# Optimization experiments

Measured on AMD Instinct MI355X. Metric: run time of the kernel, lower is better.

The kernel has to match this reference:

```python
import jax, jax.numpy as jnp
import numpy as np

N, R, E, H, D_MAX = 1024, 8192, 1024, 4, 48
DH = E // H
P_EDGE = 16.0 / R  # average in-degree ~16


def setup_inputs() -> dict:
    key = jax.random.key(0)
    ks = jax.random.split(key, 6)
    s = 0.02
    return {
        "target": jax.random.normal(ks[0], (N, E), jnp.float32),
        "source": jax.random.normal(ks[1], (R, E), jnp.float32),
        "adj": (jax.random.uniform(ks[2], (N, R)) < P_EDGE).astype(jnp.float32),
        "W_trans": jax.random.normal(ks[3], (E, E), jnp.float32) * s,
        "b_trans": jnp.zeros((E,), jnp.float32),
        "in_proj_w": jax.random.normal(ks[4], (3 * E, E), jnp.float32) * s,
        "in_proj_b": jnp.zeros((3 * E,), jnp.float32),
        "out_w": jax.random.normal(ks[5], (E, E), jnp.float32) * s,
        "out_b": jnp.zeros((E,), jnp.float32),
        "unit_id": 0,
    }


def reference(target, source, adj, W_trans, b_trans, in_proj_w, in_proj_b, out_w, out_b, unit_id):
    # source = relu(trans_fc(source))
    src = jax.nn.relu(source @ W_trans.T + b_trans)  # [R, E]

    # build padded neighbor index lists (torch loops per node; here vectorized)
    deg = adj.sum(axis=1).astype(jnp.int32)                # [N]
    order = jnp.argsort(-adj, axis=1)[:, :D_MAX]           # stable: 1-columns first, ascending col idx
    valid = jnp.arange(D_MAX)[None, :] < deg[:, None]      # [N, D] True = real neighbor
    neigh = jnp.where(valid, order, 0)                     # pad with index 0 (masked, like torch)
    kv_in = src[neigh]                                     # [N, D, E] gathered neighbor feats

    # nn.MultiheadAttention: q=target (len-1 query), k=v=padded neighbors
    Wq, Wk, Wv = jnp.split(in_proj_w, 3, axis=0)
    bq, bk, bv = jnp.split(in_proj_b, 3)
    q = (target @ Wq.T + bq).reshape(-1, H, DH)            # [N, H, dh]
    k = (kv_in @ Wk.T + bk).reshape(-1, D_MAX, H, DH)      # [N, D, H, dh]
    v = (kv_in @ Wv.T + bv).reshape(-1, D_MAX, H, DH)

    scores = jnp.einsum('nhd,nkhd->nhk', q, k) / np.float32(np.sqrt(DH))  # [N, H, D]
    # key_padding_mask: padded slots -> -inf; give zero-degree nodes one dummy
    # unmasked slot so softmax stays finite (their output is zeroed below)
    safe_valid = valid.at[:, 0].set(valid[:, 0] | (deg == 0))
    scores = jnp.where(safe_valid[:, None, :], scores, -jnp.inf)
    attn = jax.nn.softmax(scores, axis=-1)
    out = jnp.einsum('nhk,nkhd->nhd', attn, v).reshape(-1, E)
    out = out @ out_w.T + out_b

    # scatter back: inactive (degree-0) nodes stay zero, like att_res_padded
    return jnp.where((deg > 0)[:, None], out, jnp.zeros((), out.dtype))
```

## Files before the change

### kernel.cpp

```cpp
#include <hip/hip_runtime.h>

#define N_NODES 1024
#define R_SRC   8192
#define E_DIM   1024
#define H_HEADS 4
#define DH_DIM  256
#define D_MAXN  48

typedef __attribute__((ext_vector_type(8))) short short8;
typedef __attribute__((ext_vector_type(4))) float f32x4;

__device__ __forceinline__ unsigned short f2bf(float f) {
    unsigned u = __float_as_uint(f);
    unsigned r = u + 0x7fffu + ((u >> 16) & 1u);
    return (unsigned short)(r >> 16);
}
__device__ __forceinline__ float bf2f(unsigned short b) {
    return __uint_as_float(((unsigned)b) << 16);
}
__device__ __forceinline__ void gload16(const void* g, void* l) {
    __builtin_amdgcn_global_load_lds(
        (const __attribute__((address_space(1))) unsigned int*)g,
        (__attribute__((address_space(3))) unsigned int*)l,
        16, 0, 0);
}
template<int N> __device__ __forceinline__ void vwait() {
    if constexpr (N == 8)       asm volatile("s_waitcnt vmcnt(8)" ::: "memory");
    else if constexpr (N == 6)  asm volatile("s_waitcnt vmcnt(6)" ::: "memory");
    else if constexpr (N == 1)  asm volatile("s_waitcnt vmcnt(1)" ::: "memory");
    else                        asm volatile("s_waitcnt vmcnt(0)" ::: "memory");
}

struct GD {
    const unsigned short* A;
    const unsigned short* B;
    const float* bias;
    void* C;
    int N, K, nbx, relu, outbf;
    const int* rowmask;
};

template<int BM, int BN>
__global__ __launch_bounds__(512) void gemm_t(GD d0, GD d1, int split)
{
    constexpr int AI = BM / 64;
    constexpr int BI = BN / 64;
    constexpr int VN = AI + BI;
    constexpr int FM = BM / 32;
    constexpr int FN = BN / 64;

    __shared__ __align__(16) unsigned short lds[3][(BM + BN) * 64];

    int bid = blockIdx.x;
    const int nwg = gridDim.x;
    bid = (bid & 7) * (nwg >> 3) + (bid >> 3);

    GD d; int q;
    if (bid < split) { d = d0; q = bid; }
    else             { d = d1; q = bid - split; }
    const int m0 = (q / d.nbx) * BM;
    const int n0 = (q % d.nbx) * BN;
    const int K  = d.K;

    const int t = threadIdx.x;
    const int w = t >> 6, l = t & 63;
    const int wm = w >> 2, wn = w & 3;

    const int trow = t >> 3, tkc = t & 7;
    const int tswz = tkc ^ (trow & 7);
    const unsigned short* gA[AI];
    const unsigned short* gB[BI];
#pragma unroll
    for (int i = 0; i < AI; ++i)
        gA[i] = d.A + (size_t)(m0 + i * 64 + trow) * K + tswz * 8;
#pragma unroll
    for (int i = 0; i < BI; ++i)
        gB[i] = d.B + (size_t)(n0 + i * 64 + trow) * K + tswz * 8;

    f32x4 acc[FM][FN] = {};

    auto STAGE = [&](int c, int kt) {
        const int ko = kt * 64;
#pragma unroll
        for (int i = 0; i < AI; ++i)
            gload16(gA[i] + ko, &lds[c][(i * 512 + t) * 8]);
#pragma unroll
        for (int i = 0; i < BI; ++i)
            gload16(gB[i] + ko, &lds[c][BM * 64 + (i * 512 + t) * 8]);
    };

    const int nt = K / 64;
    STAGE(0, 0);
    STAGE(1, 1);
    vwait<VN>();
    __builtin_amdgcn_s_barrier();

    const int lr = l & 15, hi = l >> 4;
    const int rsw = l & 7;
    const int cs0 = ((0 + hi) ^ rsw) * 8;
    const int cs1 = ((4 + hi) ^ rsw) * 8;
    const int abase = (wm * (BM / 2) + lr) * 64;
    const int bbase = BM * 64 + (wn * 64 + lr) * 64;

    for (int kt = 0; kt < nt; ++kt) {
        const int cur = kt % 3;
        if (kt + 2 < nt) STAGE((kt + 2) % 3, kt + 2);

        const unsigned short* Ls = &lds[cur][0];

        short8 bv[FN][2];
#pragma unroll
        for (int fj = 0; fj < FN; ++fj) {
            bv[fj][0] = *(const short8*)&Ls[bbase + fj * 1024 + cs0];
            bv[fj][1] = *(const short8*)&Ls[bbase + fj * 1024 + cs1];
        }
#pragma unroll
        for (int g = 0; g < FM; g += 4) {
            short8 av[4][2];
#pragma unroll
            for (int fi = 0; fi < 4; ++fi) {
                av[fi][0] = *(const short8*)&Ls[abase + (g + fi) * 1024 + cs0];
                av[fi][1] = *(const short8*)&Ls[abase + (g + fi) * 1024 + cs1];
            }
            __builtin_amdgcn_s_setprio(1);
#pragma unroll
            for (int ks = 0; ks < 2; ++ks)
#pragma unroll
                for (int fi = 0; fi < 4; ++fi)
#pragma unroll
                    for (int fj = 0; fj < FN; ++fj)
                        acc[g + fi][fj] = __builtin_amdgcn_mfma_f32_16x16x32_bf16(
                            av[fi][ks], bv[fj][ks], acc[g + fi][fj], 0, 0, 0);
            __builtin_amdgcn_s_setprio(0);
        }

        asm volatile("" ::: "memory");
        __builtin_amdgcn_s_barrier();
        if (kt + 2 < nt) {
            vwait<VN>();
        } else {
            vwait<0>();
        }
        __builtin_amdgcn_s_barrier();
    }

#pragma unroll
    for (int fj = 0; fj < FN; ++fj) {
        const int c = n0 + wn * 64 + fj * 16 + lr;
        const float bvs = d.bias[c];
#pragma unroll
        for (int fi = 0; fi < FM; ++fi) {
            const int rb = m0 + wm * (BM / 2) + fi * 16 + hi * 4;
#pragma unroll
            for (int qq = 0; qq < 4; ++qq) {
                const int r = rb + qq;
                float x = acc[fi][fj][qq] + bvs;
                if (d.relu) x = fmaxf(x, 0.0f);
                if (d.rowmask && d.rowmask[r] == 0) x = 0.0f;
                if (d.outbf) ((unsigned short*)d.C)[(size_t)r * d.N + c] = f2bf(x);
                else         ((float*)d.C)[(size_t)r * d.N + c] = x;
            }
        }
    }
}

struct GS {
    const unsigned short* A;
    const unsigned short* B;
    const float* bias;
    void* C;
    int lda, ldb, ldc, K, relu, outbf;
    long long azs, bzs, czs;
    int bias_zs;
    const int* rowmask;
};

__global__ __launch_bounds__(256) void gemm_s(GS g)
{
    const int z = blockIdx.z;
    const unsigned short* A = g.A + (size_t)((long long)z * g.azs);
    const unsigned short* B = g.B + (size_t)((long long)z * g.bzs);
    const float* bias = g.bias ? g.bias + (size_t)z * g.bias_zs : nullptr;

    __shared__ __align__(16) unsigned short S[128 * 32];

    const int t = threadIdx.x;
    const int m0 = blockIdx.y * 64;
    const int n0 = blockIdx.x * 64;
    const int w = t >> 6, l = t & 63;
    const int wrow = (w >> 1) * 32;
    const int wcol = (w & 1) * 32;
    const int lr = l & 15;
    const int kg = (l >> 4) * 8;

    f32x4 acc[2][2] = {};

    const unsigned short* gp[2];
    unsigned short* lp[2];
    {
        const int c0 = t;
        gp[0] = A + (size_t)(m0 + (c0 >> 2)) * g.lda + (c0 & 3) * 8;
        lp[0] = &S[c0 * 8];
        const int c1 = t;
        gp[1] = B + (size_t)(n0 + (c1 >> 2)) * g.ldb + (c1 & 3) * 8;
        lp[1] = &S[2048 + c1 * 8];
    }

    for (int k0 = 0; k0 < g.K; k0 += 32) {
        gload16(gp[0] + k0, lp[0]);
        gload16(gp[1] + k0, lp[1]);
        __syncthreads();

        short8 af[2], bw[2];
#pragma unroll
        for (int i = 0; i < 2; ++i)
            af[i] = *(const short8*)&S[(wrow + i * 16 + lr) * 32 + kg];
#pragma unroll
        for (int j = 0; j < 2; ++j)
            bw[j] = *(const short8*)&S[2048 + (wcol + j * 16 + lr) * 32 + kg];
#pragma unroll
        for (int i = 0; i < 2; ++i)
#pragma unroll
            for (int j = 0; j < 2; ++j)
                acc[i][j] = __builtin_amdgcn_mfma_f32_16x16x32_bf16(
                    af[i], bw[j], acc[i][j], 0, 0, 0);
        __syncthreads();
    }

#pragma unroll
    for (int j = 0; j < 2; ++j) {
        const int c = n0 + wcol + j * 16 + lr;
        const float bv = bias ? bias[c] : 0.0f;
#pragma unroll
        for (int i = 0; i < 2; ++i) {
            const int rbase = m0 + wrow + i * 16 + (l >> 4) * 4;
#pragma unroll
            for (int qq = 0; qq < 4; ++qq) {
                const int r = rbase + qq;
                float x = acc[i][j][qq] + bv;
                if (g.relu) x = fmaxf(x, 0.0f);
                if (g.rowmask && g.rowmask[r] == 0) x = 0.0f;
                if (g.outbf)
                    ((unsigned short*)g.C)[(size_t)((long long)z * g.czs) + (size_t)r * g.ldc + c] = f2bf(x);
                else
                    ((float*)g.C)[(size_t)((long long)z * g.czs) + (size_t)r * g.ldc + c] = x;
            }
        }
    }
}

struct ConvArgs {
    const float* s[4];
    unsigned short* d[4];
    unsigned off[5];
};

__global__ __launch_bounds__(256) void pre_kernel(
    const float* __restrict__ adj, int* __restrict__ neigh, int* __restrict__ deg,
    ConvArgs a, const float* __restrict__ inw_f, const float* __restrict__ tgt_f,
    const float* __restrict__ in_b, unsigned short* __restrict__ WkT,
    unsigned short* __restrict__ Q_bf, int nconv)
{
    __shared__ __align__(16) unsigned char smem[64 * 65 * 4];
    const int t = threadIdx.x;

    if (blockIdx.x < 256) {
        unsigned short (*QS)[64 * 32] = (unsigned short (*)[64 * 32])smem;
        const int qb = blockIdx.x;
        const int m0 = (qb >> 4) * 64;
        const int n0 = (qb & 15) * 64;
        const int w = t >> 6, l = t & 63;
        const int wrow = (w >> 1) * 32;
        const int wcol = (w & 1) * 32;
        const int lr = l & 15;
        const int kg = (l >> 4) * 8;
        const int row = t >> 2, k8 = (t & 3) * 8;

        const float* ga = tgt_f + (size_t)(m0 + row) * E_DIM + k8;
        const float* gb = inw_f + (size_t)(n0 + row) * E_DIM + k8;

        f32x4 acc[2][2] = {};

        for (int k0 = 0; k0 < E_DIM; k0 += 32) {
            float4 a0 = *(const float4*)(ga + k0);
            float4 a1 = *(const float4*)(ga + k0 + 4);
            float4 b0 = *(const float4*)(gb + k0);
            float4 b1 = *(const float4*)(gb + k0 + 4);
            short8 av, bv;
            av[0] = (short)f2bf(a0.x); av[1] = (short)f2bf(a0.y);
            av[2] = (short)f2bf(a0.z); av[3] = (short)f2bf(a0.w);
            av[4] = (short)f2bf(a1.x); av[5] = (short)f2bf(a1.y);
            av[6] = (short)f2bf(a1.z); av[7] = (short)f2bf(a1.w);
            bv[0] = (short)f2bf(b0.x); bv[1] = (short)f2bf(b0.y);
            bv[2] = (short)f2bf(b0.z); bv[3] = (short)f2bf(b0.w);
            bv[4] = (short)f2bf(b1.x); bv[5] = (short)f2bf(b1.y);
            bv[6] = (short)f2bf(b1.z); bv[7] = (short)f2bf(b1.w);
            *(short8*)&QS[0][row * 32 + k8] = av;
            *(short8*)&QS[1][row * 32 + k8] = bv;
            __syncthreads();

            short8 af[2], bw[2];
#pragma unroll
            for (int i = 0; i < 2; ++i)
                af[i] = *(const short8*)&QS[0][(wrow + i * 16 + lr) * 32 + kg];
#pragma unroll
            for (int j = 0; j < 2; ++j)
                bw[j] = *(const short8*)&QS[1][(wcol + j * 16 + lr) * 32 + kg];
#pragma unroll
            for (int i = 0; i < 2; ++i)
#pragma unroll
                for (int j = 0; j < 2; ++j)
                    acc[i][j] = __builtin_amdgcn_mfma_f32_16x16x32_bf16(
                        af[i], bw[j], acc[i][j], 0, 0, 0);
            __syncthreads();
        }

#pragma unroll
        for (int j = 0; j < 2; ++j) {
            const int c = n0 + wcol + j * 16 + lr;
            const float bv = in_b[c];
#pragma unroll
            for (int i = 0; i < 2; ++i) {
                const int rbase = m0 + wrow + i * 16 + (l >> 4) * 4;
#pragma unroll
                for (int qq = 0; qq < 4; ++qq)
                    Q_bf[(size_t)(rbase + qq) * E_DIM + c] = f2bf(acc[i][j][qq] + bv);
            }
        }
        return;
    }

    if (blockIdx.x < 512) {
        float (*tile)[65] = (float (*)[65])smem;
        const int tb = blockIdx.x - 256;
        const int h = tb >> 6, rem = tb & 63;
        const int e0 = (rem >> 2) * 64, d0 = (rem & 3) * 64;
        const int r = t >> 2, c4 = (t & 3) * 16;
        const float* tsrc = inw_f + (size_t)(E_DIM + h * 256 + d0 + r) * E_DIM + e0 + c4;
#pragma unroll
        for (int jj = 0; jj < 4; ++jj) {
            float4 v = ((const float4*)tsrc)[jj];
            tile[r][c4 + jj * 4 + 0] = v.x;
            tile[r][c4 + jj * 4 + 1] = v.y;
            tile[r][c4 + jj * 4 + 2] = v.z;
            tile[r][c4 + jj * 4 + 3] = v.w;
        }
        __syncthreads();
        const int er = t >> 2, dc = (t & 3) * 16;
        unsigned short* wout = WkT + ((size_t)h * E_DIM + e0 + er) * 256 + d0 + dc;
#pragma unroll
        for (int jj = 0; jj < 4; ++jj) {
            ushort4 o;
            o.x = f2bf(tile[dc + jj * 4 + 0][er]);
            o.y = f2bf(tile[dc + jj * 4 + 1][er]);
            o.z = f2bf(tile[dc + jj * 4 + 2][er]);
            o.w = f2bf(tile[dc + jj * 4 + 3][er]);
            ((ushort4*)wout)[jj] = o;
        }
        return;
    }

    if (blockIdx.x < (unsigned)(512 + N_NODES)) {
        int* s_cnt = (int*)smem;
        int (*s_idx)[D_MAXN] = (int (*)[D_MAXN])(smem + 16);

        const int n    = blockIdx.x - 512;
        const int w    = t >> 6;
        const int lane = t & 63;
        const float* row = adj + (size_t)n * R_SRC;

        const int seg0 = w * (R_SRC / 4);
        const unsigned long long lower = (1ULL << lane) - 1ULL;
        int total = 0;

        for (int base = seg0; base < seg0 + R_SRC / 4; base += 256) {
            const float v0 = row[base + lane];
            const float v1 = row[base + 64 + lane];
            const float v2 = row[base + 128 + lane];
            const float v3 = row[base + 192 + lane];
            const unsigned long long m0 = __ballot(v0 != 0.0f);
            const unsigned long long m1 = __ballot(v1 != 0.0f);
            const unsigned long long m2 = __ballot(v2 != 0.0f);
            const unsigned long long m3 = __ballot(v3 != 0.0f);
            int p;
            p = total + __popcll(m0 & lower);
            if (v0 != 0.0f && p < D_MAXN) s_idx[w][p] = base + lane;
            total += __popcll(m0);
            p = total + __popcll(m1 & lower);
            if (v1 != 0.0f && p < D_MAXN) s_idx[w][p] = base + 64 + lane;
            total += __popcll(m1);
            p = total + __popcll(m2 & lower);
            if (v2 != 0.0f && p < D_MAXN) s_idx[w][p] = base + 128 + lane;
            total += __popcll(m2);
            p = total + __popcll(m3 & lower);
            if (v3 != 0.0f && p < D_MAXN) s_idx[w][p] = base + 192 + lane;
            total += __popcll(m3);
        }
        if (lane == 0) s_cnt[w] = total;
        __syncthreads();

        int start = 0;
#pragma unroll
        for (int i = 0; i < 4; ++i) if (i < w) start += s_cnt[i];
        const int degree = s_cnt[0] + s_cnt[1] + s_cnt[2] + s_cnt[3];
        const int nstore = total < D_MAXN ? total : D_MAXN;
        if (lane < nstore) {
            const int gpos = start + lane;
            if (gpos < D_MAXN) neigh[n * D_MAXN + gpos] = s_idx[w][lane];
        }
        if (t == 0) deg[n] = degree;
        return;
    }

    unsigned i = (blockIdx.x - 512 - N_NODES) * 256 + t;
    if (i >= a.off[4]) return;
    int seg = 0;
#pragma unroll
    for (int s = 1; s < 4; ++s) seg += (i >= a.off[s]);
    unsigned j = i - a.off[seg];
    float4 v = ((const float4*)a.s[seg])[j];
    ushort4 o;
    o.x = f2bf(v.x); o.y = f2bf(v.y); o.z = f2bf(v.z); o.w = f2bf(v.w);
    ((ushort4*)a.d[seg])[j] = o;
}

__global__ __launch_bounds__(256) void gather_ctx(
    const float* __restrict__ Ahat, const unsigned short* __restrict__ srcrel,
    const int* __restrict__ neigh, const int* __restrict__ deg,
    unsigned short* __restrict__ ctx)
{
    const int n = blockIdx.x;
    const int t = threadIdx.x;
    const int h = t >> 6;
    const int lane = t & 63;

    unsigned short* crow = ctx + ((size_t)n * H_HEADS + h) * E_DIM + lane * 16;
    const int degree = deg[n];
    if (degree == 0) {
        ushort4 z4 = {0, 0, 0, 0};
#pragma unroll
        for (int j = 0; j < 4; ++j) ((ushort4*)crow)[j] = z4;
        return;
    }
    const int dv = degree < D_MAXN ? degree : D_MAXN;

    __shared__ int s_neigh[D_MAXN];
    if (t < dv) s_neigh[t] = neigh[n * D_MAXN + t];
    __syncthreads();

    float a[16];
    {
        const float4* ap = (const float4*)(Ahat + (size_t)n * (H_HEADS * E_DIM) + h * E_DIM + lane * 16);
#pragma unroll
        for (int j = 0; j < 4; ++j) {
            float4 v = ap[j];
            a[j * 4 + 0] = v.x; a[j * 4 + 1] = v.y; a[j * 4 + 2] = v.z; a[j * 4 + 3] = v.w;
        }
    }

    float m = -3.4e38f, sum = 0.0f;
    float cacc[16];
#pragma unroll
    for (int i = 0; i < 16; ++i) cacc[i] = 0.0f;

    const float scale = 0.0625f;

    int d = 0;
    for (; d + 1 < dv; d += 2) {
        const ushort4* rp0 = (const ushort4*)(srcrel + (size_t)s_neigh[d]     * E_DIM + lane * 16);
        const ushort4* rp1 = (const ushort4*)(srcrel + (size_t)s_neigh[d + 1] * E_DIM + lane * 16);
        ushort4 w00 = rp0[0], w01 = rp0[1], w02 = rp0[2], w03 = rp0[3];
        ushort4 w10 = rp1[0], w11 = rp1[1], w12 = rp1[2], w13 = rp1[3];
        float e0[16], e1[16];
        e0[0]=bf2f(w00.x); e0[1]=bf2f(w00.y); e0[2]=bf2f(w00.z); e0[3]=bf2f(w00.w);
        e0[4]=bf2f(w01.x); e0[5]=bf2f(w01.y); e0[6]=bf2f(w01.z); e0[7]=bf2f(w01.w);
        e0[8]=bf2f(w02.x); e0[9]=bf2f(w02.y); e0[10]=bf2f(w02.z); e0[11]=bf2f(w02.w);
        e0[12]=bf2f(w03.x); e0[13]=bf2f(w03.y); e0[14]=bf2f(w03.z); e0[15]=bf2f(w03.w);
        e1[0]=bf2f(w10.x); e1[1]=bf2f(w10.y); e1[2]=bf2f(w10.z); e1[3]=bf2f(w10.w);
        e1[4]=bf2f(w11.x); e1[5]=bf2f(w11.y); e1[6]=bf2f(w11.z); e1[7]=bf2f(w11.w);
        e1[8]=bf2f(w12.x); e1[9]=bf2f(w12.y); e1[10]=bf2f(w12.z); e1[11]=bf2f(w12.w);
        e1[12]=bf2f(w13.x); e1[13]=bf2f(w13.y); e1[14]=bf2f(w13.z); e1[15]=bf2f(w13.w);

        float s0 = 0.0f, s1 = 0.0f;
#pragma unroll
        for (int i = 0; i < 16; ++i) { s0 = fmaf(a[i], e0[i], s0); s1 = fmaf(a[i], e1[i], s1); }
#pragma unroll
        for (int off = 32; off > 0; off >>= 1) {
            s0 += __shfl_xor(s0, off);
            s1 += __shfl_xor(s1, off);
        }
        s0 *= scale; s1 *= scale;

        if (s0 > m) {
            const float f = __expf(m - s0);
            sum *= f;
#pragma unroll
            for (int i = 0; i < 16; ++i) cacc[i] *= f;
            m = s0;
        }
        {
            const float wgt = __expf(s0 - m);
            sum += wgt;
#pragma unroll
            for (int i = 0; i < 16; ++i) cacc[i] = fmaf(wgt, e0[i], cacc[i]);
        }
        if (s1 > m) {
            const float f = __expf(m - s1);
            sum *= f;
#pragma unroll
            for (int i = 0; i < 16; ++i) cacc[i] *= f;
            m = s1;
        }
        {
            const float wgt = __expf(s1 - m);
            sum += wgt;
#pragma unroll
            for (int i = 0; i < 16; ++i) cacc[i] = fmaf(wgt, e1[i], cacc[i]);
        }
    }
    for (; d < dv; ++d) {
        const ushort4* rp = (const ushort4*)(srcrel + (size_t)s_neigh[d] * E_DIM + lane * 16);
        float e[16];
#pragma unroll
        for (int j = 0; j < 4; ++j) {
            ushort4 v = rp[j];
            e[j * 4 + 0] = bf2f(v.x); e[j * 4 + 1] = bf2f(v.y);
            e[j * 4 + 2] = bf2f(v.z); e[j * 4 + 3] = bf2f(v.w);
        }
        float s = 0.0f;
#pragma unroll
        for (int i = 0; i < 16; ++i) s = fmaf(a[i], e[i], s);
#pragma unroll
        for (int off = 32; off > 0; off >>= 1) s += __shfl_xor(s, off);
        s *= scale;
        if (s > m) {
            const float f = __expf(m - s);
            sum *= f;
#pragma unroll
            for (int i = 0; i < 16; ++i) cacc[i] *= f;
            m = s;
        }
        const float wgt = __expf(s - m);
        sum += wgt;
#pragma unroll
        for (int i = 0; i < 16; ++i) cacc[i] = fmaf(wgt, e[i], cacc[i]);
    }

    const float inv = 1.0f / sum;
#pragma unroll
    for (int j = 0; j < 4; ++j) {
        ushort4 o;
        o.x = f2bf(cacc[j * 4 + 0] * inv);
        o.y = f2bf(cacc[j * 4 + 1] * inv);
        o.z = f2bf(cacc[j * 4 + 2] * inv);
        o.w = f2bf(cacc[j * 4 + 3] * inv);
        ((ushort4*)crow)[j] = o;
    }
}

extern "C" void kernel_launch(void* const* d_in, const int* in_sizes, int n_in,
                              void* d_out, int out_size, void* d_ws, size_t ws_size,
                              hipStream_t stream)
{
    const float* target  = (const float*)d_in[0];
    const float* source  = (const float*)d_in[1];
    const float* adj     = (const float*)d_in[2];
    const float* W_trans = (const float*)d_in[3];
    const float* b_trans = (const float*)d_in[4];
    const float* in_w    = (const float*)d_in[5];
    const float* in_b    = (const float*)d_in[6];
    const float* out_w   = (const float*)d_in[7];
    const float* out_b   = (const float*)d_in[8];
    float* out = (float*)d_out;

    char* ws = (char*)d_ws;
    unsigned short* src_bf    = (unsigned short*)ws; ws += (size_t)R_SRC * E_DIM * 2;
    unsigned short* wt_bf     = (unsigned short*)ws; ws += (size_t)E_DIM * E_DIM * 2;
    unsigned short* wv_bf     = (unsigned short*)ws; ws += (size_t)E_DIM * E_DIM * 2;
    unsigned short* outw_bf   = (unsigned short*)ws; ws += (size_t)E_DIM * E_DIM * 2;
    unsigned short* srcrel_bf = (unsigned short*)ws; ws += (size_t)R_SRC * E_DIM * 2;
    unsigned short* WkT_bf    = (unsigned short*)ws; ws += (size_t)H_HEADS * E_DIM * DH_DIM * 2;
    unsigned short* Q_bf      = (unsigned short*)ws; ws += (size_t)N_NODES * E_DIM * 2;
    float*          Ahat      = (float*)ws;         ws += (size_t)N_NODES * H_HEADS * E_DIM * 4;
    unsigned short* ctx_bf    = (unsigned short*)ws; ws += (size_t)N_NODES * H_HEADS * E_DIM * 2;
    unsigned short* attn_bf   = (unsigned short*)ws; ws += (size_t)N_NODES * E_DIM * 2;
    int*            neigh     = (int*)ws;            ws += (size_t)N_NODES * D_MAXN * 4;
    int*            deg       = (int*)ws;            ws += (size_t)N_NODES * 4;

    const size_t EE = (size_t)E_DIM * E_DIM;

    {
        ConvArgs a;
        const unsigned sz4[4] = {
            (unsigned)((size_t)R_SRC * E_DIM / 4),
            (unsigned)(EE / 4),
            (unsigned)(EE / 4),
            (unsigned)(EE / 4)};
        a.s[0] = source;        a.d[0] = src_bf;
        a.s[1] = W_trans;       a.d[1] = wt_bf;
        a.s[2] = in_w + 2 * EE; a.d[2] = wv_bf;
        a.s[3] = out_w;         a.d[3] = outw_bf;
        a.off[0] = 0;
        for (int i = 0; i < 4; ++i) a.off[i + 1] = a.off[i] + sz4[i];
        const int nconv = (int)((a.off[4] + 255) / 256);
        pre_kernel<<<512 + N_NODES + nconv, 256, 0, stream>>>(
            adj, neigh, deg, a, in_w, target, in_b, WkT_bf, Q_bf, nconv);
    }

    {
        GD ds;
        ds.A = src_bf; ds.B = wt_bf; ds.bias = b_trans; ds.C = srcrel_bf;
        ds.N = E_DIM; ds.K = E_DIM; ds.nbx = E_DIM / 256; ds.relu = 1; ds.outbf = 1;
        ds.rowmask = nullptr;
        const int sblocks = (R_SRC / 128) * (E_DIM / 256);
        gemm_t<128, 256><<<sblocks, 512, 0, stream>>>(ds, ds, sblocks);
    }

    {
        GS g;
        g.A = Q_bf; g.B = WkT_bf; g.bias = nullptr; g.C = Ahat;
        g.lda = E_DIM; g.ldb = DH_DIM; g.ldc = H_HEADS * E_DIM; g.K = DH_DIM;
        g.relu = 0; g.outbf = 0;
        g.azs = DH_DIM;
        g.bzs = (long long)E_DIM * DH_DIM;
        g.czs = E_DIM;
        g.bias_zs = 0; g.rowmask = nullptr;
        gemm_s<<<dim3(E_DIM / 64, N_NODES / 64, H_HEADS), 256, 0, stream>>>(g);
    }

    gather_ctx<<<N_NODES, 256, 0, stream>>>(Ahat, srcrel_bf, neigh, deg, ctx_bf);

    {
        GS g;
        g.A = ctx_bf; g.B = wv_bf; g.bias = in_b + 2 * E_DIM; g.C = attn_bf;
        g.lda = H_HEADS * E_DIM; g.ldb = E_DIM; g.ldc = E_DIM; g.K = E_DIM;
        g.relu = 0; g.outbf = 1;
        g.azs = E_DIM;
        g.bzs = (long long)DH_DIM * E_DIM;
        g.czs = DH_DIM;
        g.bias_zs = DH_DIM; g.rowmask = nullptr;
        gemm_s<<<dim3(DH_DIM / 64, N_NODES / 64, H_HEADS), 256, 0, stream>>>(g);
    }

    {
        GS g;
        g.A = attn_bf; g.B = outw_bf; g.bias = out_b; g.C = out;
        g.lda = E_DIM; g.ldb = E_DIM; g.ldc = E_DIM; g.K = E_DIM;
        g.relu = 0; g.outbf = 0; g.azs = 0; g.bzs = 0; g.czs = 0; g.bias_zs = 0;
        g.rowmask = deg;
        gemm_s<<<dim3(E_DIM / 64, N_NODES / 64, 1), 256, 0, stream>>>(g);
    }
}
```

Baseline: 114.4 us.

## Prefetch next K-tile into registers and swizzle LDS in Q projection

The Q-projection branch of pre_kernel now uses a 64-wide K step instead of 32 and loads the next tile's fp32 inputs into registers while the current tile is converted and multiplied. LDS stores and loads use an XOR swizzle on 16-byte chunks to avoid bank conflicts in the wider rows. This is meant to hide global load latency and halve the number of barriers per K, at the cost of more registers for the prefetch buffers.

```diff
diff --git a/kernel.cpp b/kernel.cpp
--- a/kernel.cpp
+++ b/kernel.cpp
@@ -265,7 +265,7 @@
     const int t = threadIdx.x;
 
     if (blockIdx.x < 256) {
-        unsigned short (*QS)[64 * 32] = (unsigned short (*)[64 * 32])smem;
+        unsigned short (*QS)[64 * 64] = (unsigned short (*)[64 * 64])smem;
         const int qb = blockIdx.x;
         const int m0 = (qb >> 4) * 64;
         const int n0 = (qb & 15) * 64;
@@ -273,46 +273,79 @@
         const int wrow = (w >> 1) * 32;
         const int wcol = (w & 1) * 32;
         const int lr = l & 15;
-        const int kg = (l >> 4) * 8;
-        const int row = t >> 2, k8 = (t & 3) * 8;
-
-        const float* ga = tgt_f + (size_t)(m0 + row) * E_DIM + k8;
-        const float* gb = inw_f + (size_t)(n0 + row) * E_DIM + k8;
+        const int hi = l >> 4;
+        const int rsw = lr & 7;
+
+        const int row = t >> 2, kq = t & 3;
+        const float* ga = tgt_f + (size_t)(m0 + row) * E_DIM + kq * 16;
+        const float* gb = inw_f + (size_t)(n0 + row) * E_DIM + kq * 16;
 
         f32x4 acc[2][2] = {};
 
-        for (int k0 = 0; k0 < E_DIM; k0 += 32) {
-            float4 a0 = *(const float4*)(ga + k0);
-            float4 a1 = *(const float4*)(ga + k0 + 4);
-            float4 b0 = *(const float4*)(gb + k0);
-            float4 b1 = *(const float4*)(gb + k0 + 4);
-            short8 av, bv;
-            av[0] = (short)f2bf(a0.x); av[1] = (short)f2bf(a0.y);
-            av[2] = (short)f2bf(a0.z); av[3] = (short)f2bf(a0.w);
-            av[4] = (short)f2bf(a1.x); av[5] = (short)f2bf(a1.y);
-            av[6] = (short)f2bf(a1.z); av[7] = (short)f2bf(a1.w);
-            bv[0] = (short)f2bf(b0.x); bv[1] = (short)f2bf(b0.y);
-            bv[2] = (short)f2bf(b0.z); bv[3] = (short)f2bf(b0.w);
-            bv[4] = (short)f2bf(b1.x); bv[5] = (short)f2bf(b1.y);
-            bv[6] = (short)f2bf(b1.z); bv[7] = (short)f2bf(b1.w);
-            *(short8*)&QS[0][row * 32 + k8] = av;
-            *(short8*)&QS[1][row * 32 + k8] = bv;
+        float4 pa[4], pb[4], na[4], nb[4];
+#pragma unroll
+        for (int j = 0; j < 4; ++j) {
+            pa[j] = *(const float4*)(ga + j * 4);
+            pb[j] = *(const float4*)(gb + j * 4);
+        }
+
+        for (int k0 = 0; k0 < E_DIM; k0 += 64) {
+            if (k0 + 64 < E_DIM) {
+#pragma unroll
+                for (int j = 0; j < 4; ++j) {
+                    na[j] = *(const float4*)(ga + k0 + 64 + j * 4);
+                    nb[j] = *(const float4*)(gb + k0 + 64 + j * 4);
+                }
+            }
+            short8 sa0, sa1, sb0, sb1;
+            sa0[0]=(short)f2bf(pa[0].x); sa0[1]=(short)f2bf(pa[0].y);
+            sa0[2]=(short)f2bf(pa[0].z); sa0[3]=(short)f2bf(pa[0].w);
+            sa0[4]=(short)f2bf(pa[1].x); sa0[5]=(short)f2bf(pa[1].y);
+            sa0[6]=(short)f2bf(pa[1].z); sa0[7]=(short)f2bf(pa[1].w);
+            sa1[0]=(short)f2bf(pa[2].x); sa1[1]=(short)f2bf(pa[2].y);
+            sa1[2]=(short)f2bf(pa[2].z); sa1[3]=(short)f2bf(pa[2].w);
+            sa1[4]=(short)f2bf(pa[3].x); sa1[5]=(short)f2bf(pa[3].y);
+            sa1[6]=(short)f2bf(pa[3].z); sa1[7]=(short)f2bf(pa[3].w);
+            sb0[0]=(short)f2bf(pb[0].x); sb0[1]=(short)f2bf(pb[0].y);
+            sb0[2]=(short)f2bf(pb[0].z); sb0[3]=(short)f2bf(pb[0].w);
+            sb0[4]=(short)f2bf(pb[1].x); sb0[5]=(short)f2bf(pb[1].y);
+            sb0[6]=(short)f2bf(pb[1].z); sb0[7]=(short)f2bf(pb[1].w);
+            sb1[0]=(short)f2bf(pb[2].x); sb1[1]=(short)f2bf(pb[2].y);
+            sb1[2]=(short)f2bf(pb[2].z); sb1[3]=(short)f2bf(pb[2].w);
+            sb1[4]=(short)f2bf(pb[3].x); sb1[5]=(short)f2bf(pb[3].y);
+            sb1[6]=(short)f2bf(pb[3].z); sb1[7]=(short)f2bf(pb[3].w);
+
             __syncthreads();
-
-            short8 af[2], bw[2];
-#pragma unroll
-            for (int i = 0; i < 2; ++i)
-                af[i] = *(const short8*)&QS[0][(wrow + i * 16 + lr) * 32 + kg];
-#pragma unroll
-            for (int j = 0; j < 2; ++j)
-                bw[j] = *(const short8*)&QS[1][(wcol + j * 16 + lr) * 32 + kg];
-#pragma unroll
-            for (int i = 0; i < 2; ++i)
-#pragma unroll
-                for (int j = 0; j < 2; ++j)
-                    acc[i][j] = __builtin_amdgcn_mfma_f32_16x16x32_bf16(
-                        af[i], bw[j], acc[i][j], 0, 0, 0);
+            const int rs = row & 7;
+            *(short8*)&QS[0][row * 64 + ((2 * kq + 0) ^ rs) * 8] = sa0;
+            *(short8*)&QS[0][row * 64 + ((2 * kq + 1) ^ rs) * 8] = sa1;
+            *(short8*)&QS[1][row * 64 + ((2 * kq + 0) ^ rs) * 8] = sb0;
+            *(short8*)&QS[1][row * 64 + ((2 * kq + 1) ^ rs) * 8] = sb1;
             __syncthreads();
+
+#pragma unroll
+            for (int ks = 0; ks < 2; ++ks) {
+                short8 af[2], bw[2];
+#pragma unroll
+                for (int i = 0; i < 2; ++i) {
+                    const int rr = wrow + i * 16 + lr;
+                    af[i] = *(const short8*)&QS[0][rr * 64 + ((ks * 4 + hi) ^ rsw) * 8];
+                }
+#pragma unroll
+                for (int j = 0; j < 2; ++j) {
+                    const int rr = wcol + j * 16 + lr;
+                    bw[j] = *(const short8*)&QS[1][rr * 64 + ((ks * 4 + hi) ^ rsw) * 8];
+                }
+#pragma unroll
+                for (int i = 0; i < 2; ++i)
+#pragma unroll
+                    for (int j = 0; j < 2; ++j)
+                        acc[i][j] = __builtin_amdgcn_mfma_f32_16x16x32_bf16(
+                            af[i], bw[j], acc[i][j], 0, 0, 0);
+            }
+
+#pragma unroll
+            for (int j = 0; j < 4; ++j) { pa[j] = na[j]; pb[j] = nb[j]; }
         }
 
 #pragma unroll
```

Result: no change. 116.2 us (+1.6%).
